# Kernel optimization log

Measured on AMD Instinct MI355X. Metric: run time of the kernel, lower is better.

The kernel has to match this reference:

```python
import jax, jax.numpy as jnp
import numpy as np

NUM_NODES = 100000
NUM_EDGES = 600000
NUM_GRAPHS = 1000
EMB = 128


def setup_inputs() -> dict:
    key = jax.random.key(0)
    ks = jax.random.split(key, 12)
    x = jax.random.normal(ks[0], (NUM_NODES, 4), dtype=jnp.float32)
    edge_index = jax.random.randint(ks[1], (2, NUM_EDGES), 0, NUM_NODES, dtype=jnp.int32)
    x_scalar = jax.random.normal(ks[2], (NUM_GRAPHS, 4), dtype=jnp.float32)
    batch_index = jnp.sort(jax.random.randint(ks[3], (NUM_NODES,), 0, NUM_GRAPHS, dtype=jnp.int32))
    def glorot(k, shape):
        fan_in, fan_out = shape[0], shape[1]
        s = jnp.sqrt(2.0 / (fan_in + fan_out)).astype(jnp.float32)
        return jax.random.normal(k, shape, dtype=jnp.float32) * s
    return {
        "x": x,
        "edge_index": edge_index,
        "x_scalar": x_scalar,
        "batch_index": batch_index,
        "W0": glorot(ks[4], (4, EMB)), "b0": jnp.zeros((EMB,), jnp.float32),
        "W1": glorot(ks[5], (EMB, EMB)), "b1": jnp.zeros((EMB,), jnp.float32),
        "W2": glorot(ks[6], (EMB, EMB)), "b2": jnp.zeros((EMB,), jnp.float32),
        "W3": glorot(ks[7], (EMB, EMB)), "b3": jnp.zeros((EMB,), jnp.float32),
        "Wl1": glorot(ks[8], (EMB + 4, 64)), "bl1": jnp.zeros((64,), jnp.float32),
        "Wl2": glorot(ks[9], (64, 1)), "bl2": jnp.zeros((1,), jnp.float32),
    }


def _gcn_norm(edge_index, num_nodes):
    # PyG GCNConv default: add self-loops, symmetric normalization
    loop = jnp.arange(num_nodes, dtype=edge_index.dtype)
    src = jnp.concatenate([edge_index[0], loop])
    dst = jnp.concatenate([edge_index[1], loop])
    deg = jax.ops.segment_sum(jnp.ones_like(src, dtype=jnp.float32), dst,
                              num_segments=num_nodes)
    dinv = jnp.where(deg > 0, jax.lax.rsqrt(jnp.maximum(deg, 1e-12)), 0.0)
    norm = dinv[src] * dinv[dst]  # [E+N]
    return src, dst, norm


def _gcn_conv(h, src, dst, norm, W, b, num_nodes):
    h = h @ W                                   # [N, out]
    msg = h[src] * norm[:, None]                # gather + normalize
    out = jax.ops.segment_sum(msg, dst, num_segments=num_nodes)  # scatter-add
    return out + b


def reference(x, edge_index, x_scalar, batch_index,
              W0, b0, W1, b1, W2, b2, W3, b3, Wl1, bl1, Wl2, bl2):
    n = x.shape[0]
    src, dst, norm = _gcn_norm(edge_index, n)
    h = jax.nn.relu(_gcn_conv(x, src, dst, norm, W0, b0, n))
    h = jax.nn.relu(_gcn_conv(h, src, dst, norm, W1, b1, n))
    h = jax.nn.relu(_gcn_conv(h, src, dst, norm, W2, b2, n))
    h = jax.nn.relu(_gcn_conv(h, src, dst, norm, W3, b3, n))
    # global mean pool over batch_index
    sums = jax.ops.segment_sum(h, batch_index, num_segments=NUM_GRAPHS)
    cnts = jax.ops.segment_sum(jnp.ones((n,), jnp.float32), batch_index,
                               num_segments=NUM_GRAPHS)
    pooled = sums / jnp.maximum(cnts, 1.0)[:, None]          # [G, EMB]
    feat = jnp.concatenate([pooled, x_scalar], axis=1)       # [G, EMB+4]
    out = jax.nn.relu(feat @ Wl1 + bl1) @ Wl2 + bl2          # [G, 1]
    return out
```

## Files before the change

kernel.cpp:

```cpp
#include <hip/hip_runtime.h>

#define NN 100000
#define EE 600000
#define GG 1000
#define NB ((NN + 255) / 256)
#define CAP 32
#define LDSPAD 136

typedef __bf16 bf16x8 __attribute__((ext_vector_type(8)));
typedef float f32x4 __attribute__((ext_vector_type(4)));
typedef unsigned int u32;

__device__ inline float2 bf2_to_f2(u32 u) {
  return make_float2(__uint_as_float(u << 16), __uint_as_float(u & 0xffff0000u));
}
__device__ inline u32 f2_to_bf2(float a, float b) {
  union { __bf16 h[2]; u32 u; } pk;
  pk.h[0] = (__bf16)a; pk.h[1] = (__bf16)b;
  return pk.u;
}


__global__ void k_init(int* cnt, int* gstart) {
  int i = blockIdx.x * 256 + threadIdx.x;
  if (i < NN) cnt[i] = 0;
  if (i <= GG) gstart[i] = NN;
}

__global__ void k_fill(const int* __restrict__ src, const int* __restrict__ dst,
                       int* cnt, int2* __restrict__ wbucket) {
  int e = blockIdx.x * 256 + threadIdx.x;
  if (e >= EE) return;
  int s = src[e], d = dst[e];
  int pos = atomicAdd(&cnt[d], 1);
  if (pos < CAP - 1) wbucket[d * CAP + pos].x = s;
}

__global__ void k_prep(const int* __restrict__ cnt, float* __restrict__ dinv,
                       const int* __restrict__ batch, int* gstart,
                       const float* __restrict__ W1, const float* __restrict__ W2,
                       const float* __restrict__ W3,
                       __bf16* __restrict__ Wt1, __bf16* __restrict__ Wt2,
                       __bf16* __restrict__ Wt3) {
  int gid = blockIdx.x * 256 + threadIdx.x;
  if (gid < NN) {
    dinv[gid] = rsqrtf((float)(cnt[gid] + 1));
    int b = batch[gid];
    if (gid == 0) {
      for (int g = 0; g <= b; ++g) gstart[g] = 0;
    } else {
      int prev = batch[gid - 1];
      for (int g = prev + 1; g <= b; ++g) gstart[g] = gid;
    }
  }
  if (gid < 3 * 16384) {
    int which = gid >> 14, idx = gid & 16383;
    int n = idx >> 7, k = idx & 127;
    const float* W = (which == 0) ? W1 : (which == 1) ? W2 : W3;
    __bf16* Wt = (which == 0) ? Wt1 : (which == 1) ? Wt2 : Wt3;
    Wt[(size_t)n * 128 + k] = (__bf16)W[(size_t)k * 128 + n];
  }
}

__global__ void k_wb(const int* __restrict__ cnt, const float* __restrict__ dinv,
                     int2* __restrict__ wbucket) {
  int gid = blockIdx.x * 256 + threadIdx.x;
  if (gid >= NN * CAP) return;
  int d = gid >> 5, slot = gid & 31;
  int m = min(cnt[d], CAP - 1);
  int mp = (m + 4) & ~3;
  if (slot >= mp) return;
  float dd = dinv[d];
  int s; float w;
  if (slot < m)      { s = wbucket[gid].x; w = dinv[s] * dd; }
  else if (slot == m){ s = d;              w = dd * dd; }
  else               { s = d;              w = 0.f; }
  wbucket[gid] = make_int2(s, __float_as_int(w));
}

__global__ void k_l0(const float4* __restrict__ x, const int* __restrict__ cnt,
                     const int2* __restrict__ wbucket,
                     const float* __restrict__ W0, const float* __restrict__ b0,
                     u32* __restrict__ hout2) {
  int gid = blockIdx.x * 256 + threadIdx.x;
  if (gid >= NN * 16) return;
  int node = gid >> 4, cg = gid & 15;
  int m1 = min(cnt[node], CAP - 1) + 1;
  float4 yv = make_float4(0.f, 0.f, 0.f, 0.f);
  for (int e = 0; e < m1; ++e) {
    int2 md = wbucket[(size_t)node * CAP + e];
    float wgt = __int_as_float(md.y);
    float4 v = x[md.x];
    yv.x = fmaf(wgt, v.x, yv.x);
    yv.y = fmaf(wgt, v.y, yv.y);
    yv.z = fmaf(wgt, v.z, yv.z);
    yv.w = fmaf(wgt, v.w, yv.w);
  }
  float v[8];
  #pragma unroll
  for (int k = 0; k < 2; ++k) {
    float4 b = *(const float4*)(b0 + cg * 8 + k * 4);
    v[k * 4 + 0] = b.x; v[k * 4 + 1] = b.y; v[k * 4 + 2] = b.z; v[k * 4 + 3] = b.w;
  }
  #pragma unroll
  for (int k = 0; k < 4; ++k) {
    float yk = (k == 0) ? yv.x : (k == 1) ? yv.y : (k == 2) ? yv.z : yv.w;
    float4 wa = *(const float4*)(W0 + k * 128 + cg * 8);
    float4 wb = *(const float4*)(W0 + k * 128 + cg * 8 + 4);
    v[0] = fmaf(yk, wa.x, v[0]); v[1] = fmaf(yk, wa.y, v[1]);
    v[2] = fmaf(yk, wa.z, v[2]); v[3] = fmaf(yk, wa.w, v[3]);
    v[4] = fmaf(yk, wb.x, v[4]); v[5] = fmaf(yk, wb.y, v[5]);
    v[6] = fmaf(yk, wb.z, v[6]); v[7] = fmaf(yk, wb.w, v[7]);
  }
  uint4 o;
  o.x = f2_to_bf2(fmaxf(v[0], 0.f), fmaxf(v[1], 0.f));
  o.y = f2_to_bf2(fmaxf(v[2], 0.f), fmaxf(v[3], 0.f));
  o.z = f2_to_bf2(fmaxf(v[4], 0.f), fmaxf(v[5], 0.f));
  o.w = f2_to_bf2(fmaxf(v[6], 0.f), fmaxf(v[7], 0.f));
  *(uint4*)(hout2 + (size_t)node * 64 + cg * 4) = o;
}

__global__ __launch_bounds__(256) void k_agg23(const __bf16* __restrict__ hlin,
                                               const int* __restrict__ cnt,
                                               const int2* __restrict__ wbucket,
                                               u32* __restrict__ hout2) {
  int wid = (blockIdx.x * 4) + (threadIdx.x >> 6);
  int lane = threadIdx.x & 63;
  int ln = lane & 15, quad = lane >> 4;
  int na = wid * 2, nb = wid * 2 + 1;
  if (na >= NN) return;

  int nodeL = (lane < 32) ? na : nb;
  int2 me = make_int2(0, 0);
  if (nodeL < NN) me = wbucket[(size_t)nodeL * CAP + (lane & 31)];
  int s_l = me.x, w_l = me.y;
  int mpa = (min(cnt[na], CAP - 1) + 4) & ~3;
  int mpb = (nb < NN) ? ((min(cnt[nb], CAP - 1) + 4) & ~3) : 0;
  int mpmin = min(mpa, mpb);

  float aa[8] = {0.f, 0.f, 0.f, 0.f, 0.f, 0.f, 0.f, 0.f};
  float ab[8] = {0.f, 0.f, 0.f, 0.f, 0.f, 0.f, 0.f, 0.f};

  int j = 0;
  for (; j + 8 <= mpmin; j += 8) {
    int p0 = (j + quad) * 4, p1 = (j + 4 + quad) * 4;
    int sa0 = __builtin_amdgcn_ds_bpermute(p0, s_l);
    int sa1 = __builtin_amdgcn_ds_bpermute(p1, s_l);
    int sb0 = __builtin_amdgcn_ds_bpermute(128 + p0, s_l);
    int sb1 = __builtin_amdgcn_ds_bpermute(128 + p1, s_l);
    float wa0 = __int_as_float(__builtin_amdgcn_ds_bpermute(p0, w_l));
    float wa1 = __int_as_float(__builtin_amdgcn_ds_bpermute(p1, w_l));
    float wb0 = __int_as_float(__builtin_amdgcn_ds_bpermute(128 + p0, w_l));
    float wb1 = __int_as_float(__builtin_amdgcn_ds_bpermute(128 + p1, w_l));
    uint4 ua0 = *(const uint4*)(hlin + ((size_t)sa0 << 7) + ln * 8);
    uint4 ua1 = *(const uint4*)(hlin + ((size_t)sa1 << 7) + ln * 8);
    uint4 ub0 = *(const uint4*)(hlin + ((size_t)sb0 << 7) + ln * 8);
    uint4 ub1 = *(const uint4*)(hlin + ((size_t)sb1 << 7) + ln * 8);
    float2 f;
    f = bf2_to_f2(ua0.x); aa[0] = fmaf(wa0, f.x, aa[0]); aa[1] = fmaf(wa0, f.y, aa[1]);
    f = bf2_to_f2(ua0.y); aa[2] = fmaf(wa0, f.x, aa[2]); aa[3] = fmaf(wa0, f.y, aa[3]);
    f = bf2_to_f2(ua0.z); aa[4] = fmaf(wa0, f.x, aa[4]); aa[5] = fmaf(wa0, f.y, aa[5]);
    f = bf2_to_f2(ua0.w); aa[6] = fmaf(wa0, f.x, aa[6]); aa[7] = fmaf(wa0, f.y, aa[7]);
    f = bf2_to_f2(ua1.x); aa[0] = fmaf(wa1, f.x, aa[0]); aa[1] = fmaf(wa1, f.y, aa[1]);
    f = bf2_to_f2(ua1.y); aa[2] = fmaf(wa1, f.x, aa[2]); aa[3] = fmaf(wa1, f.y, aa[3]);
    f = bf2_to_f2(ua1.z); aa[4] = fmaf(wa1, f.x, aa[4]); aa[5] = fmaf(wa1, f.y, aa[5]);
    f = bf2_to_f2(ua1.w); aa[6] = fmaf(wa1, f.x, aa[6]); aa[7] = fmaf(wa1, f.y, aa[7]);
    f = bf2_to_f2(ub0.x); ab[0] = fmaf(wb0, f.x, ab[0]); ab[1] = fmaf(wb0, f.y, ab[1]);
    f = bf2_to_f2(ub0.y); ab[2] = fmaf(wb0, f.x, ab[2]); ab[3] = fmaf(wb0, f.y, ab[3]);
    f = bf2_to_f2(ub0.z); ab[4] = fmaf(wb0, f.x, ab[4]); ab[5] = fmaf(wb0, f.y, ab[5]);
    f = bf2_to_f2(ub0.w); ab[6] = fmaf(wb0, f.x, ab[6]); ab[7] = fmaf(wb0, f.y, ab[7]);
    f = bf2_to_f2(ub1.x); ab[0] = fmaf(wb1, f.x, ab[0]); ab[1] = fmaf(wb1, f.y, ab[1]);
    f = bf2_to_f2(ub1.y); ab[2] = fmaf(wb1, f.x, ab[2]); ab[3] = fmaf(wb1, f.y, ab[3]);
    f = bf2_to_f2(ub1.z); ab[4] = fmaf(wb1, f.x, ab[4]); ab[5] = fmaf(wb1, f.y, ab[5]);
    f = bf2_to_f2(ub1.w); ab[6] = fmaf(wb1, f.x, ab[6]); ab[7] = fmaf(wb1, f.y, ab[7]);
  }
  if (j < mpmin) {
    int p = (j + quad) * 4;
    int sa = __builtin_amdgcn_ds_bpermute(p, s_l);
    int sb = __builtin_amdgcn_ds_bpermute(128 + p, s_l);
    float wa = __int_as_float(__builtin_amdgcn_ds_bpermute(p, w_l));
    float wb = __int_as_float(__builtin_amdgcn_ds_bpermute(128 + p, w_l));
    uint4 ua = *(const uint4*)(hlin + ((size_t)sa << 7) + ln * 8);
    uint4 ub = *(const uint4*)(hlin + ((size_t)sb << 7) + ln * 8);
    float2 f;
    f = bf2_to_f2(ua.x); aa[0] = fmaf(wa, f.x, aa[0]); aa[1] = fmaf(wa, f.y, aa[1]);
    f = bf2_to_f2(ua.y); aa[2] = fmaf(wa, f.x, aa[2]); aa[3] = fmaf(wa, f.y, aa[3]);
    f = bf2_to_f2(ua.z); aa[4] = fmaf(wa, f.x, aa[4]); aa[5] = fmaf(wa, f.y, aa[5]);
    f = bf2_to_f2(ua.w); aa[6] = fmaf(wa, f.x, aa[6]); aa[7] = fmaf(wa, f.y, aa[7]);
    f = bf2_to_f2(ub.x); ab[0] = fmaf(wb, f.x, ab[0]); ab[1] = fmaf(wb, f.y, ab[1]);
    f = bf2_to_f2(ub.y); ab[2] = fmaf(wb, f.x, ab[2]); ab[3] = fmaf(wb, f.y, ab[3]);
    f = bf2_to_f2(ub.z); ab[4] = fmaf(wb, f.x, ab[4]); ab[5] = fmaf(wb, f.y, ab[5]);
    f = bf2_to_f2(ub.w); ab[6] = fmaf(wb, f.x, ab[6]); ab[7] = fmaf(wb, f.y, ab[7]);
    j += 4;
  }
  for (; j < mpa; j += 4) {
    int p = (j + quad) * 4;
    int s0 = __builtin_amdgcn_ds_bpermute(p, s_l);
    float w0 = __int_as_float(__builtin_amdgcn_ds_bpermute(p, w_l));
    uint4 u0 = *(const uint4*)(hlin + ((size_t)s0 << 7) + ln * 8);
    float2 f;
    f = bf2_to_f2(u0.x); aa[0] = fmaf(w0, f.x, aa[0]); aa[1] = fmaf(w0, f.y, aa[1]);
    f = bf2_to_f2(u0.y); aa[2] = fmaf(w0, f.x, aa[2]); aa[3] = fmaf(w0, f.y, aa[3]);
    f = bf2_to_f2(u0.z); aa[4] = fmaf(w0, f.x, aa[4]); aa[5] = fmaf(w0, f.y, aa[5]);
    f = bf2_to_f2(u0.w); aa[6] = fmaf(w0, f.x, aa[6]); aa[7] = fmaf(w0, f.y, aa[7]);
  }
  for (; j < mpb; j += 4) {
    int p = 128 + (j + quad) * 4;
    int s0 = __builtin_amdgcn_ds_bpermute(p, s_l);
    float w0 = __int_as_float(__builtin_amdgcn_ds_bpermute(p, w_l));
    uint4 u0 = *(const uint4*)(hlin + ((size_t)s0 << 7) + ln * 8);
    float2 f;
    f = bf2_to_f2(u0.x); ab[0] = fmaf(w0, f.x, ab[0]); ab[1] = fmaf(w0, f.y, ab[1]);
    f = bf2_to_f2(u0.y); ab[2] = fmaf(w0, f.x, ab[2]); ab[3] = fmaf(w0, f.y, ab[3]);
    f = bf2_to_f2(u0.z); ab[4] = fmaf(w0, f.x, ab[4]); ab[5] = fmaf(w0, f.y, ab[5]);
    f = bf2_to_f2(u0.w); ab[6] = fmaf(w0, f.x, ab[6]); ab[7] = fmaf(w0, f.y, ab[7]);
  }

  #pragma unroll
  for (int k = 0; k < 8; ++k) {
    aa[k] += __shfl_xor(aa[k], 16); aa[k] += __shfl_xor(aa[k], 32);
    ab[k] += __shfl_xor(ab[k], 16); ab[k] += __shfl_xor(ab[k], 32);
  }
  if (quad == 0) {
    uint4 oa;
    oa.x = f2_to_bf2(aa[0], aa[1]); oa.y = f2_to_bf2(aa[2], aa[3]);
    oa.z = f2_to_bf2(aa[4], aa[5]); oa.w = f2_to_bf2(aa[6], aa[7]);
    *(uint4*)(hout2 + (size_t)na * 64 + ln * 4) = oa;
    if (nb < NN) {
      uint4 ob;
      ob.x = f2_to_bf2(ab[0], ab[1]); ob.y = f2_to_bf2(ab[2], ab[3]);
      ob.z = f2_to_bf2(ab[4], ab[5]); ob.w = f2_to_bf2(ab[6], ab[7]);
      *(uint4*)(hout2 + (size_t)nb * 64 + ln * 4) = ob;
    }
  }
}

__global__ __launch_bounds__(256) void k_mfma(const __bf16* __restrict__ hin,
                                              const __bf16* __restrict__ Wt,
                                              const float* __restrict__ bias,
                                              __bf16* __restrict__ hout) {
  __shared__ __bf16 As[128 * LDSPAD];
  int tid = threadIdx.x;
  int row0 = blockIdx.x * 128;
  int lane = tid & 63, w = tid >> 6;
  int ln = lane & 15, quad = lane >> 4;

  bf16x8 bfrag[8][4];
  float bcol[8];
  #pragma unroll
  for (int nt = 0; nt < 8; ++nt) {
    bcol[nt] = bias[nt * 16 + ln];
    #pragma unroll
    for (int kc = 0; kc < 4; ++kc)
      bfrag[nt][kc] = *(const bf16x8*)(Wt + (size_t)(nt * 16 + ln) * 128 + kc * 32 + quad * 8);
  }

  #pragma unroll
  for (int i = 0; i < 8; ++i) {
    int eb = (i * 256 + tid) * 8;
    int r = eb >> 7, c = eb & 127;
    int gr = row0 + r;
    uint4 v = make_uint4(0, 0, 0, 0);
    if (gr < NN) v = *(const uint4*)(hin + (size_t)gr * 128 + c);
    *(uint4*)&As[r * LDSPAD + c] = v;
  }
  __syncthreads();

  f32x4 acc[2][8];
  #pragma unroll
  for (int rt = 0; rt < 2; ++rt)
    #pragma unroll
    for (int nt = 0; nt < 8; ++nt) acc[rt][nt] = (f32x4){0.f, 0.f, 0.f, 0.f};

  #pragma unroll
  for (int kc = 0; kc < 4; ++kc) {
    bf16x8 a0 = *(const bf16x8*)&As[(w * 32 + ln) * LDSPAD + kc * 32 + quad * 8];
    bf16x8 a1 = *(const bf16x8*)&As[(w * 32 + 16 + ln) * LDSPAD + kc * 32 + quad * 8];
    #pragma unroll
    for (int nt = 0; nt < 8; ++nt) {
      acc[0][nt] = __builtin_amdgcn_mfma_f32_16x16x32_bf16(a0, bfrag[nt][kc], acc[0][nt], 0, 0, 0);
      acc[1][nt] = __builtin_amdgcn_mfma_f32_16x16x32_bf16(a1, bfrag[nt][kc], acc[1][nt], 0, 0, 0);
    }
  }

  #pragma unroll
  for (int rt = 0; rt < 2; ++rt)
    #pragma unroll
    for (int nt = 0; nt < 8; ++nt)
      #pragma unroll
      for (int reg = 0; reg < 4; ++reg) {
        int gr = row0 + w * 32 + rt * 16 + quad * 4 + reg;
        if (gr < NN)
          hout[(size_t)gr * 128 + nt * 16 + ln] =
              (__bf16)fmaxf(acc[rt][nt][reg] + bcol[nt], 0.f);
      }
}

__global__ __launch_bounds__(256) void k_poolmlp(const uint2* __restrict__ h4u,
                                                 const int* __restrict__ gstart,
                                                 const float* __restrict__ xs,
                                                 const float* __restrict__ Wl1,
                                                 const float* __restrict__ bl1,
                                                 const float* __restrict__ Wl2,
                                                 const float* __restrict__ bl2,
                                                 float* __restrict__ out) {
  __shared__ float4 part[8][32];
  __shared__ float pooled[128];
  int g = blockIdx.x;
  int beg = gstart[g], end = gstart[g + 1];
  int tid = threadIdx.x;
  int cg = tid & 31;
  int rg = tid >> 5;
  float4 acc = make_float4(0.f, 0.f, 0.f, 0.f);
  for (int i = beg + rg; i < end; i += 8) {
    uint2 u = h4u[(size_t)i * 32 + cg];
    acc.x += __uint_as_float(u.x << 16);
    acc.y += __uint_as_float(u.x & 0xffff0000u);
    acc.z += __uint_as_float(u.y << 16);
    acc.w += __uint_as_float(u.y & 0xffff0000u);
  }
  part[rg][cg] = acc;
  __syncthreads();
  if (tid < 32) {
    float4 s = part[0][tid];
    #pragma unroll
    for (int r = 1; r < 8; ++r) {
      float4 v = part[r][tid];
      s.x += v.x; s.y += v.y; s.z += v.z; s.w += v.w;
    }
    float sc = 1.f / fmaxf((float)(end - beg), 1.f);
    pooled[tid * 4 + 0] = s.x * sc;
    pooled[tid * 4 + 1] = s.y * sc;
    pooled[tid * 4 + 2] = s.z * sc;
    pooled[tid * 4 + 3] = s.w * sc;
  }
  __syncthreads();
  if (tid < 64) {
    float hj = bl1[tid];
    #pragma unroll 4
    for (int k = 0; k < 128; ++k) hj = fmaf(pooled[k], Wl1[k * 64 + tid], hj);
    const float* xr = xs + g * 4;
    #pragma unroll
    for (int k = 0; k < 4; ++k) hj = fmaf(xr[k], Wl1[(128 + k) * 64 + tid], hj);
    hj = fmaxf(hj, 0.f);
    float val = hj * Wl2[tid];
    #pragma unroll
    for (int off = 32; off > 0; off >>= 1) val += __shfl_down(val, off);
    if (tid == 0) out[g] = val + bl2[0];
  }
}


extern "C" void kernel_launch(void* const* d_in, const int* in_sizes, int n_in,
                              void* d_out, int out_size, void* d_ws, size_t ws_size,
                              hipStream_t stream) {
  const float* x    = (const float*)d_in[0];
  const int*   ei   = (const int*)d_in[1];
  const float* xs   = (const float*)d_in[2];
  const int*   batch= (const int*)d_in[3];
  const float* W0   = (const float*)d_in[4];
  const float* b0   = (const float*)d_in[5];
  const float* W1   = (const float*)d_in[6];
  const float* b1   = (const float*)d_in[7];
  const float* W2   = (const float*)d_in[8];
  const float* b2   = (const float*)d_in[9];
  const float* W3   = (const float*)d_in[10];
  const float* b3   = (const float*)d_in[11];
  const float* Wl1  = (const float*)d_in[12];
  const float* bl1  = (const float*)d_in[13];
  const float* Wl2  = (const float*)d_in[14];
  const float* bl2  = (const float*)d_in[15];
  const int* srcA = ei;
  const int* dstA = ei + EE;
  float* out = (float*)d_out;

  char* p = (char*)d_ws;
  auto take = [&](size_t bytes) { char* q = p; p += (bytes + 255) & ~(size_t)255; return q; };
  __bf16* hA    = (__bf16*)take((size_t)NN * 128 * 2);
  __bf16* hB    = (__bf16*)take((size_t)NN * 128 * 2);
  int*    cnt   = (int*)take((size_t)NN * 4);
  float*  dinv  = (float*)take((size_t)NN * 4);
  int2*   wbucket = (int2*)take((size_t)NN * CAP * 8);
  int*    gstart= (int*)take((size_t)(GG + 1) * 4);
  __bf16* Wt1   = (__bf16*)take(16384 * 2);
  __bf16* Wt2   = (__bf16*)take(16384 * 2);
  __bf16* Wt3   = (__bf16*)take(16384 * 2);

  k_init<<<NB, 256, 0, stream>>>(cnt, gstart);
  k_fill<<<(EE + 255) / 256, 256, 0, stream>>>(srcA, dstA, cnt, wbucket);
  k_prep<<<NB, 256, 0, stream>>>(cnt, dinv, batch, gstart, W1, W2, W3, Wt1, Wt2, Wt3);
  k_wb<<<(NN * CAP + 255) / 256, 256, 0, stream>>>(cnt, dinv, wbucket);

  k_l0<<<(NN * 16 + 255) / 256, 256, 0, stream>>>((const float4*)x, cnt, wbucket, W0, b0, (u32*)hA);
  k_agg23<<<(NN + 7) / 8, 256, 0, stream>>>(hA, cnt, wbucket, (u32*)hB);
  k_mfma<<<(NN + 127) / 128, 256, 0, stream>>>(hB, Wt1, b1, hA);
  k_agg23<<<(NN + 7) / 8, 256, 0, stream>>>(hA, cnt, wbucket, (u32*)hB);
  k_mfma<<<(NN + 127) / 128, 256, 0, stream>>>(hB, Wt2, b2, hA);
  k_agg23<<<(NN + 7) / 8, 256, 0, stream>>>(hA, cnt, wbucket, (u32*)hB);
  k_mfma<<<(NN + 127) / 128, 256, 0, stream>>>(hB, Wt3, b3, hA);

  k_poolmlp<<<GG, 256, 0, stream>>>((const uint2*)hA, gstart, xs, Wl1, bl1, Wl2, bl2, out);
}
```

Before: 356.9 us.

## Fuse mean-pool into last MFMA layer via atomics and merge prep kernels

The last GEMM layer now sums ReLU outputs directly into per-graph fp32 accumulators with atomics, using a warp-reduced fast path when a 16-row tile belongs to one graph. This removes the bf16 write and re-read of the final node features and leaves a slim head kernel that only runs the MLP. The dinv buffer is dropped by recomputing rsqrt from counts, and k_prep is merged into k_wb, saving a launch. k_agg23 also skips loading wbucket slots beyond the padded count. Pooling now accumulates in fp32 from unrounded values with nondeterministic atomic order.

```diff
diff --git a/kernel.cpp b/kernel.cpp
--- a/kernel.cpp
+++ b/kernel.cpp
@@ -3,9 +3,9 @@
 #define NN 100000
 #define EE 600000
 #define GG 1000
-#define NB ((NN + 255) / 256)
 #define CAP 32
 #define LDSPAD 136
+#define INITB ((GG * 128 + 255) / 256)
 
 typedef __bf16 bf16x8 __attribute__((ext_vector_type(8)));
 typedef float f32x4 __attribute__((ext_vector_type(4)));
@@ -21,10 +21,11 @@
 }
 
 
-__global__ void k_init(int* cnt, int* gstart) {
+__global__ void k_init(int* cnt, int* gstart, float* sums) {
   int i = blockIdx.x * 256 + threadIdx.x;
   if (i < NN) cnt[i] = 0;
   if (i <= GG) gstart[i] = NN;
+  if (i < GG * 128) sums[i] = 0.f;
 }
 
 __global__ void k_fill(const int* __restrict__ src, const int* __restrict__ dst,
@@ -36,15 +37,21 @@
   if (pos < CAP - 1) wbucket[d * CAP + pos].x = s;
 }
 
-__global__ void k_prep(const int* __restrict__ cnt, float* __restrict__ dinv,
-                       const int* __restrict__ batch, int* gstart,
-                       const float* __restrict__ W1, const float* __restrict__ W2,
-                       const float* __restrict__ W3,
-                       __bf16* __restrict__ Wt1, __bf16* __restrict__ Wt2,
-                       __bf16* __restrict__ Wt3) {
+__global__ void k_wb(const int* __restrict__ cnt, const int* __restrict__ batch,
+                     int* gstart,
+                     const float* __restrict__ W1, const float* __restrict__ W2,
+                     const float* __restrict__ W3,
+                     __bf16* __restrict__ Wt1, __bf16* __restrict__ Wt2,
+                     __bf16* __restrict__ Wt3, int2* __restrict__ wbucket) {
   int gid = blockIdx.x * 256 + threadIdx.x;
+  if (gid < 3 * 16384) {
+    int which = gid >> 14, idx = gid & 16383;
+    int n = idx >> 7, k = idx & 127;
+    const float* W = (which == 0) ? W1 : (which == 1) ? W2 : W3;
+    __bf16* Wt = (which == 0) ? Wt1 : (which == 1) ? Wt2 : Wt3;
+    Wt[(size_t)n * 128 + k] = (__bf16)W[(size_t)k * 128 + n];
+  }
   if (gid < NN) {
-    dinv[gid] = rsqrtf((float)(cnt[gid] + 1));
     int b = batch[gid];
     if (gid == 0) {
       for (int g = 0; g <= b; ++g) gstart[g] = 0;
@@ -53,29 +60,19 @@
       for (int g = prev + 1; g <= b; ++g) gstart[g] = gid;
     }
   }
-  if (gid < 3 * 16384) {
-    int which = gid >> 14, idx = gid & 16383;
-    int n = idx >> 7, k = idx & 127;
-    const float* W = (which == 0) ? W1 : (which == 1) ? W2 : W3;
-    __bf16* Wt = (which == 0) ? Wt1 : (which == 1) ? Wt2 : Wt3;
-    Wt[(size_t)n * 128 + k] = (__bf16)W[(size_t)k * 128 + n];
-  }
-}
-
-__global__ void k_wb(const int* __restrict__ cnt, const float* __restrict__ dinv,
-                     int2* __restrict__ wbucket) {
-  int gid = blockIdx.x * 256 + threadIdx.x;
-  if (gid >= NN * CAP) return;
-  int d = gid >> 5, slot = gid & 31;
-  int m = min(cnt[d], CAP - 1);
-  int mp = (m + 4) & ~3;
-  if (slot >= mp) return;
-  float dd = dinv[d];
-  int s; float w;
-  if (slot < m)      { s = wbucket[gid].x; w = dinv[s] * dd; }
-  else if (slot == m){ s = d;              w = dd * dd; }
-  else               { s = d;              w = 0.f; }
-  wbucket[gid] = make_int2(s, __float_as_int(w));
+  if (gid < NN * CAP) {
+    int d = gid >> 5, slot = gid & 31;
+    int m = min(cnt[d], CAP - 1);
+    int mp = (m + 4) & ~3;
+    if (slot < mp) {
+      float dd = rsqrtf((float)(cnt[d] + 1));
+      int s; float w;
+      if (slot < m)      { s = wbucket[gid].x; w = rsqrtf((float)(cnt[s] + 1)) * dd; }
+      else if (slot == m){ s = d;              w = dd * dd; }
+      else               { s = d;              w = 0.f; }
+      wbucket[gid] = make_int2(s, __float_as_int(w));
+    }
+  }
 }
 
 __global__ void k_l0(const float4* __restrict__ x, const int* __restrict__ cnt,
@@ -130,13 +127,16 @@
   int na = wid * 2, nb = wid * 2 + 1;
   if (na >= NN) return;
 
-  int nodeL = (lane < 32) ? na : nb;
-  int2 me = make_int2(0, 0);
-  if (nodeL < NN) me = wbucket[(size_t)nodeL * CAP + (lane & 31)];
-  int s_l = me.x, w_l = me.y;
   int mpa = (min(cnt[na], CAP - 1) + 4) & ~3;
   int mpb = (nb < NN) ? ((min(cnt[nb], CAP - 1) + 4) & ~3) : 0;
   int mpmin = min(mpa, mpb);
+
+  int nodeL = (lane < 32) ? na : nb;
+  int slot = lane & 31;
+  int mymp = (lane < 32) ? mpa : mpb;
+  int2 me = make_int2(0, 0);
+  if (slot < mymp) me = wbucket[(size_t)nodeL * CAP + slot];
+  int s_l = me.x, w_l = me.y;
 
   float aa[8] = {0.f, 0.f, 0.f, 0.f, 0.f, 0.f, 0.f, 0.f};
   float ab[8] = {0.f, 0.f, 0.f, 0.f, 0.f, 0.f, 0.f, 0.f};
@@ -296,58 +296,115 @@
       }
 }
 
-__global__ __launch_bounds__(256) void k_poolmlp(const uint2* __restrict__ h4u,
-                                                 const int* __restrict__ gstart,
-                                                 const float* __restrict__ xs,
-                                                 const float* __restrict__ Wl1,
-                                                 const float* __restrict__ bl1,
-                                                 const float* __restrict__ Wl2,
-                                                 const float* __restrict__ bl2,
-                                                 float* __restrict__ out) {
-  __shared__ float4 part[8][32];
-  __shared__ float pooled[128];
-  int g = blockIdx.x;
+__global__ __launch_bounds__(256) void k_mfma_pool(const __bf16* __restrict__ hin,
+                                                   const __bf16* __restrict__ Wt,
+                                                   const float* __restrict__ bias,
+                                                   const int* __restrict__ batch,
+                                                   float* __restrict__ sums) {
+  __shared__ __bf16 As[128 * LDSPAD];
+  int tid = threadIdx.x;
+  int row0 = blockIdx.x * 128;
+  int lane = tid & 63, w = tid >> 6;
+  int ln = lane & 15, quad = lane >> 4;
+
+  bf16x8 bfrag[8][4];
+  float bcol[8];
+  #pragma unroll
+  for (int nt = 0; nt < 8; ++nt) {
+    bcol[nt] = bias[nt * 16 + ln];
+    #pragma unroll
+    for (int kc = 0; kc < 4; ++kc)
+      bfrag[nt][kc] = *(const bf16x8*)(Wt + (size_t)(nt * 16 + ln) * 128 + kc * 32 + quad * 8);
+  }
+
+  #pragma unroll
+  for (int i = 0; i < 8; ++i) {
+    int eb = (i * 256 + tid) * 8;
+    int r = eb >> 7, c = eb & 127;
+    int gr = row0 + r;
+    uint4 v = make_uint4(0, 0, 0, 0);
+    if (gr < NN) v = *(const uint4*)(hin + (size_t)gr * 128 + c);
+    *(uint4*)&As[r * LDSPAD + c] = v;
+  }
+  __syncthreads();
+
+  f32x4 acc[2][8];
+  #pragma unroll
+  for (int rt = 0; rt < 2; ++rt)
+    #pragma unroll
+    for (int nt = 0; nt < 8; ++nt) acc[rt][nt] = (f32x4){0.f, 0.f, 0.f, 0.f};
+
+  #pragma unroll
+  for (int kc = 0; kc < 4; ++kc) {
+    bf16x8 a0 = *(const bf16x8*)&As[(w * 32 + ln) * LDSPAD + kc * 32 + quad * 8];
+    bf16x8 a1 = *(const bf16x8*)&As[(w * 32 + 16 + ln) * LDSPAD + kc * 32 + quad * 8];
+    #pragma unroll
+    for (int nt = 0; nt < 8; ++nt) {
+      acc[0][nt] = __builtin_amdgcn_mfma_f32_16x16x32_bf16(a0, bfrag[nt][kc], acc[0][nt], 0, 0, 0);
+      acc[1][nt] = __builtin_amdgcn_mfma_f32_16x16x32_bf16(a1, bfrag[nt][kc], acc[1][nt], 0, 0, 0);
+    }
+  }
+
+  #pragma unroll
+  for (int rt = 0; rt < 2; ++rt) {
+    int tr0 = row0 + w * 32 + rt * 16;
+    int trL = tr0 + 15;
+    bool uni = (trL < NN) && (batch[tr0] == batch[trL]);
+    if (uni) {
+      int b0 = batch[tr0];
+      #pragma unroll
+      for (int nt = 0; nt < 8; ++nt) {
+        float s = 0.f;
+        #pragma unroll
+        for (int reg = 0; reg < 4; ++reg)
+          s += fmaxf(acc[rt][nt][reg] + bcol[nt], 0.f);
+        s += __shfl_xor(s, 16);
+        s += __shfl_xor(s, 32);
+        if (quad == 0)
+          atomicAdd(&sums[b0 * 128 + nt * 16 + ln], s);
+      }
+    } else {
+      int bg[4]; bool ok[4];
+      #pragma unroll
+      for (int reg = 0; reg < 4; ++reg) {
+        int gr = tr0 + quad * 4 + reg;
+        ok[reg] = gr < NN;
+        bg[reg] = ok[reg] ? batch[gr] : 0;
+      }
+      #pragma unroll
+      for (int nt = 0; nt < 8; ++nt)
+        #pragma unroll
+        for (int reg = 0; reg < 4; ++reg)
+          if (ok[reg])
+            atomicAdd(&sums[bg[reg] * 128 + nt * 16 + ln],
+                      fmaxf(acc[rt][nt][reg] + bcol[nt], 0.f));
+    }
+  }
+}
+
+__global__ __launch_bounds__(64) void k_head(const float* __restrict__ sums,
+                                             const int* __restrict__ gstart,
+                                             const float* __restrict__ xs,
+                                             const float* __restrict__ Wl1,
+                                             const float* __restrict__ bl1,
+                                             const float* __restrict__ Wl2,
+                                             const float* __restrict__ bl2,
+                                             float* __restrict__ out) {
+  int g = blockIdx.x, tid = threadIdx.x;
   int beg = gstart[g], end = gstart[g + 1];
-  int tid = threadIdx.x;
-  int cg = tid & 31;
-  int rg = tid >> 5;
-  float4 acc = make_float4(0.f, 0.f, 0.f, 0.f);
-  for (int i = beg + rg; i < end; i += 8) {
-    uint2 u = h4u[(size_t)i * 32 + cg];
-    acc.x += __uint_as_float(u.x << 16);
-    acc.y += __uint_as_float(u.x & 0xffff0000u);
-    acc.z += __uint_as_float(u.y << 16);
-    acc.w += __uint_as_float(u.y & 0xffff0000u);
-  }
-  part[rg][cg] = acc;
-  __syncthreads();
-  if (tid < 32) {
-    float4 s = part[0][tid];
-    #pragma unroll
-    for (int r = 1; r < 8; ++r) {
-      float4 v = part[r][tid];
-      s.x += v.x; s.y += v.y; s.z += v.z; s.w += v.w;
-    }
-    float sc = 1.f / fmaxf((float)(end - beg), 1.f);
-    pooled[tid * 4 + 0] = s.x * sc;
-    pooled[tid * 4 + 1] = s.y * sc;
-    pooled[tid * 4 + 2] = s.z * sc;
-    pooled[tid * 4 + 3] = s.w * sc;
-  }
-  __syncthreads();
-  if (tid < 64) {
-    float hj = bl1[tid];
-    #pragma unroll 4
-    for (int k = 0; k < 128; ++k) hj = fmaf(pooled[k], Wl1[k * 64 + tid], hj);
-    const float* xr = xs + g * 4;
-    #pragma unroll
-    for (int k = 0; k < 4; ++k) hj = fmaf(xr[k], Wl1[(128 + k) * 64 + tid], hj);
-    hj = fmaxf(hj, 0.f);
-    float val = hj * Wl2[tid];
-    #pragma unroll
-    for (int off = 32; off > 0; off >>= 1) val += __shfl_down(val, off);
-    if (tid == 0) out[g] = val + bl2[0];
-  }
+  float sc = 1.f / fmaxf((float)(end - beg), 1.f);
+  float hj = bl1[tid];
+  #pragma unroll 4
+  for (int k = 0; k < 128; ++k)
+    hj = fmaf(sums[g * 128 + k] * sc, Wl1[k * 64 + tid], hj);
+  const float* xr = xs + g * 4;
+  #pragma unroll
+  for (int k = 0; k < 4; ++k) hj = fmaf(xr[k], Wl1[(128 + k) * 64 + tid], hj);
+  hj = fmaxf(hj, 0.f);
+  float val = hj * Wl2[tid];
+  #pragma unroll
+  for (int off = 32; off > 0; off >>= 1) val += __shfl_down(val, off);
+  if (tid == 0) out[g] = val + bl2[0];
 }
 
 
@@ -379,17 +436,17 @@
   __bf16* hA    = (__bf16*)take((size_t)NN * 128 * 2);
   __bf16* hB    = (__bf16*)take((size_t)NN * 128 * 2);
   int*    cnt   = (int*)take((size_t)NN * 4);
-  float*  dinv  = (float*)take((size_t)NN * 4);
   int2*   wbucket = (int2*)take((size_t)NN * CAP * 8);
   int*    gstart= (int*)take((size_t)(GG + 1) * 4);
+  float*  sums  = (float*)take((size_t)GG * 128 * 4);
   __bf16* Wt1   = (__bf16*)take(16384 * 2);
   __bf16* Wt2   = (__bf16*)take(16384 * 2);
   __bf16* Wt3   = (__bf16*)take(16384 * 2);
 
-  k_init<<<NB, 256, 0, stream>>>(cnt, gstart);
+  k_init<<<INITB, 256, 0, stream>>>(cnt, gstart, sums);
   k_fill<<<(EE + 255) / 256, 256, 0, stream>>>(srcA, dstA, cnt, wbucket);
-  k_prep<<<NB, 256, 0, stream>>>(cnt, dinv, batch, gstart, W1, W2, W3, Wt1, Wt2, Wt3);
-  k_wb<<<(NN * CAP + 255) / 256, 256, 0, stream>>>(cnt, dinv, wbucket);
+  k_wb<<<(NN * CAP + 255) / 256, 256, 0, stream>>>(cnt, batch, gstart, W1, W2, W3,
+                                                   Wt1, Wt2, Wt3, wbucket);
 
   k_l0<<<(NN * 16 + 255) / 256, 256, 0, stream>>>((const float4*)x, cnt, wbucket, W0, b0, (u32*)hA);
   k_agg23<<<(NN + 7) / 8, 256, 0, stream>>>(hA, cnt, wbucket, (u32*)hB);
@@ -397,7 +454,7 @@
   k_agg23<<<(NN + 7) / 8, 256, 0, stream>>>(hA, cnt, wbucket, (u32*)hB);
   k_mfma<<<(NN + 127) / 128, 256, 0, stream>>>(hB, Wt2, b2, hA);
   k_agg23<<<(NN + 7) / 8, 256, 0, stream>>>(hA, cnt, wbucket, (u32*)hB);
-  k_mfma<<<(NN + 127) / 128, 256, 0, stream>>>(hB, Wt3, b3, hA);
-
-  k_poolmlp<<<GG, 256, 0, stream>>>((const uint2*)hA, gstart, xs, Wl1, bl1, Wl2, bl2, out);
-}
+  k_mfma_pool<<<(NN + 127) / 128, 256, 0, stream>>>(hB, Wt3, b3, batch, sums);
+
+  k_head<<<GG, 64, 0, stream>>>(sums, gstart, xs, Wl1, bl1, Wl2, bl2, out);
+}
```

Result: slower. 367.9 us (+3.1%).
